# Performance work log

Hardware: AMD Instinct MI355X
Metric: run time of the kernel (lower is better)

The kernel has to match this reference:

```python
import jax, jax.numpy as jnp
import numpy as np

N_NODES = 50000


def gcn_conv(x, src, dst, norm, W, b, n_nodes):
    """One GCNConv layer: out = scatter_add(norm * (x @ W)[src] -> dst) + b.
    src/dst already include self loops; norm is the symmetric D^-1/2 A_hat D^-1/2 edge weight."""
    h = x @ W  # [N, C_out]
    msg = h[src] * norm[:, None]  # [E+N, C_out]
    out = jax.ops.segment_sum(msg, dst, num_segments=n_nodes)
    return out + b


def build_norm(edge_index, n_nodes):
    """Add self loops and compute symmetric GCN normalization (PyG GCNConv default)."""
    loop = jnp.arange(n_nodes, dtype=edge_index.dtype)
    src = jnp.concatenate([edge_index[0], loop])
    dst = jnp.concatenate([edge_index[1], loop])
    deg = jax.ops.segment_sum(jnp.ones_like(dst, dtype=jnp.float32), dst, num_segments=n_nodes)
    dinv = jnp.where(deg > 0, jax.lax.rsqrt(jnp.maximum(deg, 1.0)), 0.0)
    norm = dinv[src] * dinv[dst]
    return src, dst, norm


def setup_inputs() -> dict:
    key = jax.random.key(0)
    ks = jax.random.split(key, 8)
    in_c, h1, h2, out_c = 768, 256, 128, 2
    x = jax.random.normal(ks[0], (N_NODES, in_c), dtype=jnp.float32)
    edge_index = jax.random.randint(ks[1], (2, 800000), 0, N_NODES, dtype=jnp.int32)
    W1 = jax.random.normal(ks[2], (in_c, h1), dtype=jnp.float32) * 0.02
    b1 = jnp.zeros((h1,), dtype=jnp.float32)
    W2 = jax.random.normal(ks[3], (h1, h2), dtype=jnp.float32) * 0.02
    b2 = jnp.zeros((h2,), dtype=jnp.float32)
    W3 = jax.random.normal(ks[4], (h2, out_c), dtype=jnp.float32) * 0.02
    b3 = jnp.zeros((out_c,), dtype=jnp.float32)
    return {"x": x, "edge_index": edge_index, "W1": W1, "b1": b1,
            "W2": W2, "b2": b2, "W3": W3, "b3": b3}


def reference(x, edge_index, W1, b1, W2, b2, W3, b3):
    n = x.shape[0]
    src, dst, norm = build_norm(edge_index, n)
    # Dropout is identity in eval mode (training=False), so it is omitted.
    h = jax.nn.relu(gcn_conv(x, src, dst, norm, W1, b1, n))
    h = jax.nn.relu(gcn_conv(h, src, dst, norm, W2, b2, n))
    h = gcn_conv(h, src, dst, norm, W3, b3, n)
    return jax.nn.sigmoid(h)
```

## Files before the change

### kernel.cpp

```cpp
#include <hip/hip_runtime.h>
#include <math.h>

typedef short s16x8 __attribute__((ext_vector_type(8)));
typedef __bf16 b16x8 __attribute__((ext_vector_type(8)));
typedef float f32x4 __attribute__((ext_vector_type(4)));
typedef float f32x2 __attribute__((ext_vector_type(2)));
typedef unsigned int u32x4 __attribute__((ext_vector_type(4)));
typedef unsigned int u32x2 __attribute__((ext_vector_type(2)));

__device__ inline short f2bf(float f) {
    unsigned u = __float_as_uint(f);
    unsigned r = u + 0x7FFFu + ((u >> 16) & 1u);
    return (short)(r >> 16);
}
__device__ inline float bf2f(unsigned short u) {
    return __uint_as_float(((unsigned)u) << 16);
}


__global__ void count_kernel(const int* __restrict__ dst, int* __restrict__ cnt, int E) {
    int e = blockIdx.x * 256 + threadIdx.x;
    if (e < E) atomicAdd(&cnt[dst[e]], 1);
}


__device__ inline void make_wt_elem(const float* __restrict__ W, short* __restrict__ Wt,
                                    int K, int N, int idx) {
    int NB = N >> 7;
    int j = idx & 7;
    int l = (idx >> 3) & 63;
    int nt = (idx >> 9) & 7;
    int rest = idx >> 12;
    int b = rest % NB;
    int c = rest / NB;
    int k = c * 32 + (l >> 4) * 8 + j;
    int n = b * 128 + nt * 16 + (l & 15);
    Wt[idx] = f2bf(W[(size_t)k * N + n]);
}

__global__ __launch_bounds__(1024) void scanfix_kernel(
        const int* __restrict__ cnt, int* __restrict__ rp, int* __restrict__ cursor,
        float* __restrict__ dinv, int* __restrict__ bsum, int n, int E, int SB,
        const float* __restrict__ W1, short* __restrict__ Wt1,
        const float* __restrict__ W2, short* __restrict__ Wt2, int w1b) {
    int tid = threadIdx.x;
    if (blockIdx.x >= SB) {
        int b = blockIdx.x - SB;
        if (b < w1b) {
            int idx = b * 1024 + tid;
            make_wt_elem(W1, Wt1, 768, 256, idx);
        } else {
            int idx = (b - w1b) * 1024 + tid;
            make_wt_elem(W2, Wt2, 256, 128, idx);
        }
        return;
    }

    __shared__ int sdata[1024];
    __shared__ int parts[64];
    __shared__ int carry_s;
    int i = blockIdx.x * 1024 + tid;
    int v = (i < n) ? cnt[i] : 0;
    sdata[tid] = v;
    __syncthreads();
    for (int off = 1; off < 1024; off <<= 1) {
        int t = 0;
        if (tid >= off) t = sdata[tid - off];
        __syncthreads();
        sdata[tid] += t;
        __syncthreads();
    }
    if (tid == 1023)
        __hip_atomic_store(&bsum[blockIdx.x], sdata[1023] + 1,
                           __ATOMIC_RELEASE, __HIP_MEMORY_SCOPE_AGENT);
    int part = 0;
    if (tid < blockIdx.x) {
        int b;
        while ((b = __hip_atomic_load(&bsum[tid], __ATOMIC_ACQUIRE,
                                      __HIP_MEMORY_SCOPE_AGENT)) == 0) {}
        part = b - 1;
    }
    if (tid < 64) parts[tid] = part;
    __syncthreads();
    if (tid == 0) {
        int c = 0;
        for (int k = 0; k < 64; ++k) c += parts[k];
        carry_s = c;
    }
    __syncthreads();
    int r = sdata[tid] - v + carry_s;
    if (i < n) {
        rp[i] = r;
        cursor[i] = r;
        dinv[i] = rsqrtf((float)cnt[i] + 1.0f);
    }
    if (i == 0) rp[n] = E;
}


__global__ __launch_bounds__(256, 3) void gemm1_fill_kernel(
        const float* __restrict__ x, const short* __restrict__ Wt,
        unsigned char* __restrict__ h8, int M, int G1B, int FB,
        const int* __restrict__ src, const int* __restrict__ dst,
        int* __restrict__ cursor, const float* __restrict__ dinv,
        int2* __restrict__ ecw, int E) {
    constexpr int KC = 24;
    constexpr int RT = 2;
    constexpr int O = KC * 4;
    constexpr int F = KC * RT * 64 / 256;

    __shared__ s16x8 As[KC * RT * 64];

    const int tid = threadIdx.x;
    const int total = G1B + FB;
    const long long bi = (long long)blockIdx.x;
    const int fid  = (int)(bi * FB / total);
    const int fid1 = (int)((bi + 1) * FB / total);

    if (fid1 > fid) {
        int e = fid * 256 + tid;
        if (e < E) {
            int d = dst[e];
            int s = src[e];
            int p = atomicAdd(&cursor[d], 1);
            ecw[p] = make_int2(s, __float_as_int(dinv[s] * dinv[d]));
        }
        return;
    }
    const int gid = blockIdx.x - fid;

    const int m0 = gid * (RT * 16);

    s16x8 v[F];
#pragma unroll
    for (int i = 0; i < F; ++i) {
        int idx = i * 256 + tid;
        int r = idx / O;
        int o = idx - r * O;
        int row = m0 + r;
        if (row >= M) row = M - 1;
        const float4* fp = (const float4*)(x + (size_t)row * 768 + o * 8);
        float4 f0 = fp[0];
        float4 f1 = fp[1];
        u32x4 pk;
        pk.x = (__float_as_uint(f0.x) >> 16) | (__float_as_uint(f0.y) & 0xFFFF0000u);
        pk.y = (__float_as_uint(f0.z) >> 16) | (__float_as_uint(f0.w) & 0xFFFF0000u);
        pk.z = (__float_as_uint(f1.x) >> 16) | (__float_as_uint(f1.y) & 0xFFFF0000u);
        pk.w = (__float_as_uint(f1.z) >> 16) | (__float_as_uint(f1.w) & 0xFFFF0000u);
        v[i] = __builtin_bit_cast(s16x8, pk);
    }
#pragma unroll
    for (int i = 0; i < F; ++i) {
        int idx = i * 256 + tid;
        int r = idx / O;
        int o = idx - r * O;
        int c = o >> 2, q = o & 3;
        int slot = q * 16 + (((r & 15) + q + ((c & 3) << 2)) & 15);
        As[(c * RT + (r >> 4)) * 64 + slot] = v[i];
    }
    __syncthreads();

    const int lane = tid & 63;
    const int wave = tid >> 6;
    const int b128 = wave >> 1;
    const int nt0 = (wave & 1) * 4;
    const int q = lane >> 4;
    const int rl = lane & 15;
    const s16x8* wt = (const s16x8*)Wt;

    f32x4 acc[RT][4];
#pragma unroll
    for (int i = 0; i < RT; ++i)
#pragma unroll
        for (int j = 0; j < 4; ++j)
            acc[i][j] = (f32x4){0.f, 0.f, 0.f, 0.f};

#pragma unroll 4
    for (int c = 0; c < KC; ++c) {
        int slot = q * 16 + ((rl + q + ((c & 3) << 2)) & 15);
        b16x8 areg[RT], breg[4];
#pragma unroll
        for (int i = 0; i < RT; ++i)
            areg[i] = __builtin_bit_cast(b16x8, As[(c * RT + i) * 64 + slot]);
        size_t bb = (size_t)(c * 2 + b128) * 512 + nt0 * 64 + lane;
#pragma unroll
        for (int j = 0; j < 4; ++j)
            breg[j] = __builtin_bit_cast(b16x8, wt[bb + j * 64]);
#pragma unroll
        for (int i = 0; i < RT; ++i)
#pragma unroll
            for (int j = 0; j < 4; ++j)
                acc[i][j] = __builtin_amdgcn_mfma_f32_16x16x32_bf16(areg[i], breg[j], acc[i][j], 0, 0, 0);
    }

    const int quad = lane >> 4;
    const int nl = lane & 15;
#pragma unroll
    for (int i = 0; i < RT; ++i) {
        int rbase = m0 + i * 16 + quad * 4;
#pragma unroll
        for (int j = 0; j < 4; ++j) {
            int col = wave * 64 + j * 16 + nl;
#pragma unroll
            for (int r = 0; r < 4; ++r) {
                int row = rbase + r;
                if (row < M) {
                    unsigned u = __builtin_amdgcn_cvt_pk_fp8_f32(acc[i][j][r], acc[i][j][r], 0, false);
                    h8[(size_t)row * 256 + col] = (unsigned char)(u & 0xFF);
                }
            }
        }
    }
}


template<typename AT, int KC, int RT, int CW, int MINW, bool F8>
__global__ __launch_bounds__(256, MINW) void gemm_panel_kernel(
        const AT* __restrict__ A, const short* __restrict__ Wt,
        void* __restrict__ Cb, int M) {
    constexpr int K = KC * 32;
    constexpr int O = KC * 4;
    constexpr int F = KC * RT / 4;
    constexpr int NCOLS = CW * 64;
    constexpr int NB = NCOLS >> 7;
    constexpr int MT = RT * CW / 4;

    __shared__ s16x8 As[KC * RT * 64];

    const int tid = threadIdx.x;
    const int m0 = blockIdx.x * (RT * 16);

    s16x8 v[F];
#pragma unroll
    for (int i = 0; i < F; ++i) {
        int idx = i * 256 + tid;
        int r = idx / O;
        int o = idx - r * O;
        int row = m0 + r;
        if (row >= M) row = M - 1;
        v[i] = *(const s16x8*)((const unsigned short*)A + (size_t)row * K + o * 8);
    }
#pragma unroll
    for (int i = 0; i < F; ++i) {
        int idx = i * 256 + tid;
        int r = idx / O;
        int o = idx - r * O;
        int c = o >> 2, q = o & 3;
        int slot = q * 16 + (((r & 15) + q + ((c & 3) << 2)) & 15);
        As[(c * RT + (r >> 4)) * 64 + slot] = v[i];
    }
    __syncthreads();

    const int lane = tid & 63;
    const int wave = tid >> 6;
    const int cw_i = wave % CW;
    const int rg = wave / CW;
    const int mtb = rg * MT;
    const int b128 = (cw_i * 64) >> 7;
    const int nt0 = (cw_i * 4) & 7;
    const int q = lane >> 4;
    const int rl = lane & 15;
    const s16x8* wt = (const s16x8*)Wt;

    f32x4 acc[MT][4];
#pragma unroll
    for (int i = 0; i < MT; ++i)
#pragma unroll
        for (int j = 0; j < 4; ++j)
            acc[i][j] = (f32x4){0.f, 0.f, 0.f, 0.f};

#pragma unroll 4
    for (int c = 0; c < KC; ++c) {
        int slot = q * 16 + ((rl + q + ((c & 3) << 2)) & 15);
        b16x8 areg[MT], breg[4];
#pragma unroll
        for (int i = 0; i < MT; ++i)
            areg[i] = __builtin_bit_cast(b16x8, As[(c * RT + mtb + i) * 64 + slot]);
        size_t bb = (size_t)(c * NB + b128) * 512 + nt0 * 64 + lane;
#pragma unroll
        for (int j = 0; j < 4; ++j)
            breg[j] = __builtin_bit_cast(b16x8, wt[bb + j * 64]);
#pragma unroll
        for (int i = 0; i < MT; ++i)
#pragma unroll
            for (int j = 0; j < 4; ++j)
                acc[i][j] = __builtin_amdgcn_mfma_f32_16x16x32_bf16(areg[i], breg[j], acc[i][j], 0, 0, 0);
    }

    const int quad = lane >> 4;
    const int nl = lane & 15;
#pragma unroll
    for (int i = 0; i < MT; ++i) {
        int rbase = m0 + (mtb + i) * 16 + quad * 4;
#pragma unroll
        for (int j = 0; j < 4; ++j) {
            int col = cw_i * 64 + j * 16 + nl;
#pragma unroll
            for (int rr = 0; rr < 4; ++rr) {
                int row = rbase + rr;
                if (row < M) {
                    if (F8) {
                        unsigned u = __builtin_amdgcn_cvt_pk_fp8_f32(acc[i][j][rr], acc[i][j][rr], 0, false);
                        ((unsigned char*)Cb)[(size_t)row * NCOLS + col] = (unsigned char)(u & 0xFF);
                    } else {
                        ((unsigned short*)Cb)[(size_t)row * NCOLS + col] = (unsigned short)f2bf(acc[i][j][rr]);
                    }
                }
            }
        }
    }
}


__global__ __launch_bounds__(256) void agg256_f8_kernel(const unsigned char* __restrict__ h8,
                                                        const int* __restrict__ rp,
                                                        const int2* __restrict__ ecw,
                                                        const float* __restrict__ dinv,
                                                        const float* __restrict__ bias,
                                                        unsigned short* __restrict__ out, int n) {
    int node = blockIdx.x * 4 + (threadIdx.x >> 6);
    int lane = threadIdx.x & 63;
    if (node >= n) return;
    const int eg = lane >> 4;
    const int ch = lane & 15;
    float di = dinv[node];

    float acc[16];
    {
        u32x4 v = *(const u32x4*)(h8 + (size_t)node * 256 + ch * 16);
        float ws = (eg == 0) ? di * di : 0.f;
#pragma unroll
        for (int u = 0; u < 4; ++u) {
            f32x2 lo = __builtin_amdgcn_cvt_pk_f32_fp8(v[u], false);
            f32x2 hi = __builtin_amdgcn_cvt_pk_f32_fp8(v[u], true);
            acc[u * 4 + 0] = ws * lo.x; acc[u * 4 + 1] = ws * lo.y;
            acc[u * 4 + 2] = ws * hi.x; acc[u * 4 + 3] = ws * hi.y;
        }
    }

    int e0 = rp[node], e1 = rp[node + 1];
    for (int base = e0; base < e1; base += 64) {
        int idx = base + lane;
        int2 er = (idx < e1) ? ecw[idx] : make_int2(0, 0);
        int sb = er.x;
        float wb = __int_as_float(er.y);
        int cnt = e1 - base; if (cnt > 64) cnt = 64;
#pragma unroll 4
        for (int i = 0; i < cnt; i += 4) {
            int s = __shfl(sb, i + eg, 64);
            float w = __shfl(wb, i + eg, 64);
            u32x4 v = *(const u32x4*)(h8 + (size_t)s * 256 + ch * 16);
#pragma unroll
            for (int u = 0; u < 4; ++u) {
                f32x2 lo = __builtin_amdgcn_cvt_pk_f32_fp8(v[u], false);
                f32x2 hi = __builtin_amdgcn_cvt_pk_f32_fp8(v[u], true);
                acc[u * 4 + 0] += w * lo.x; acc[u * 4 + 1] += w * lo.y;
                acc[u * 4 + 2] += w * hi.x; acc[u * 4 + 3] += w * hi.y;
            }
        }
    }

#pragma unroll
    for (int k = 0; k < 16; ++k) {
        acc[k] += __shfl_xor(acc[k], 16, 64);
        acc[k] += __shfl_xor(acc[k], 32, 64);
    }

    unsigned pk[8];
#pragma unroll
    for (int k = 0; k < 8; ++k) {
        float b0 = bias[ch * 16 + 2 * k];
        float b1 = bias[ch * 16 + 2 * k + 1];
        float a0 = fmaxf(acc[2 * k] + b0, 0.f);
        float a1 = fmaxf(acc[2 * k + 1] + b1, 0.f);
        pk[k] = ((unsigned)(unsigned short)f2bf(a0)) | (((unsigned)(unsigned short)f2bf(a1)) << 16);
    }
    if (eg < 2) {
        u32x4 ov;
        ov.x = pk[eg * 4 + 0]; ov.y = pk[eg * 4 + 1];
        ov.z = pk[eg * 4 + 2]; ov.w = pk[eg * 4 + 3];
        *(u32x4*)((char*)out + (size_t)node * 512 + ch * 32 + eg * 16) = ov;
    }
}

__global__ __launch_bounds__(256) void agg128_w3_kernel(const unsigned char* __restrict__ h,
                                                        const int* __restrict__ rp,
                                                        const int2* __restrict__ ecw,
                                                        const float* __restrict__ dinv,
                                                        const float* __restrict__ b2,
                                                        const float* __restrict__ W3,
                                                        float* __restrict__ z, int n) {
    int node = blockIdx.x * 4 + (threadIdx.x >> 6);
    int lane = threadIdx.x & 63;
    if (node >= n) return;
    const int eg = lane >> 4;
    const int ch = lane & 15;
    float di = dinv[node];

    float acc[8];
    {
        u32x2 v = *(const u32x2*)(h + (size_t)node * 128 + ch * 8);
        float ws = (eg == 0) ? di * di : 0.f;
        f32x2 l0 = __builtin_amdgcn_cvt_pk_f32_fp8(v.x, false);
        f32x2 h0 = __builtin_amdgcn_cvt_pk_f32_fp8(v.x, true);
        f32x2 l1 = __builtin_amdgcn_cvt_pk_f32_fp8(v.y, false);
        f32x2 h1 = __builtin_amdgcn_cvt_pk_f32_fp8(v.y, true);
        acc[0] = ws * l0.x; acc[1] = ws * l0.y; acc[2] = ws * h0.x; acc[3] = ws * h0.y;
        acc[4] = ws * l1.x; acc[5] = ws * l1.y; acc[6] = ws * h1.x; acc[7] = ws * h1.y;
    }

    int e0 = rp[node], e1 = rp[node + 1];
    for (int base = e0; base < e1; base += 64) {
        int idx = base + lane;
        int2 er = (idx < e1) ? ecw[idx] : make_int2(0, 0);
        int sb = er.x;
        float wb = __int_as_float(er.y);
        int cnt = e1 - base; if (cnt > 64) cnt = 64;
#pragma unroll 4
        for (int i = 0; i < cnt; i += 4) {
            int s = __shfl(sb, i + eg, 64);
            float w = __shfl(wb, i + eg, 64);
            u32x2 v = *(const u32x2*)(h + (size_t)s * 128 + ch * 8);
            f32x2 l0 = __builtin_amdgcn_cvt_pk_f32_fp8(v.x, false);
            f32x2 h0 = __builtin_amdgcn_cvt_pk_f32_fp8(v.x, true);
            f32x2 l1 = __builtin_amdgcn_cvt_pk_f32_fp8(v.y, false);
            f32x2 h1 = __builtin_amdgcn_cvt_pk_f32_fp8(v.y, true);
            acc[0] += w * l0.x; acc[1] += w * l0.y; acc[2] += w * h0.x; acc[3] += w * h0.y;
            acc[4] += w * l1.x; acc[5] += w * l1.y; acc[6] += w * h1.x; acc[7] += w * h1.y;
        }
    }

#pragma unroll
    for (int k = 0; k < 8; ++k) {
        acc[k] += __shfl_xor(acc[k], 16, 64);
        acc[k] += __shfl_xor(acc[k], 32, 64);
    }

    float z0 = 0.f, z1 = 0.f;
#pragma unroll
    for (int k = 0; k < 8; ++k) {
        float a = fmaxf(acc[k] + b2[ch * 8 + k], 0.f);
        z0 += a * W3[(ch * 8 + k) * 2];
        z1 += a * W3[(ch * 8 + k) * 2 + 1];
    }
    for (int off = 8; off > 0; off >>= 1) {
        z0 += __shfl_xor(z0, off, 64);
        z1 += __shfl_xor(z1, off, 64);
    }
    if (lane == 0) {
        z[2 * (size_t)node] = z0;
        z[2 * (size_t)node + 1] = z1;
    }
}

__global__ __launch_bounds__(256) void agg3_kernel(const float* __restrict__ z,
                                                   const int* __restrict__ rp,
                                                   const int2* __restrict__ ecw,
                                                   const float* __restrict__ dinv,
                                                   const float* __restrict__ bias,
                                                   float* __restrict__ out, int n) {
    int node = blockIdx.x * 4 + (threadIdx.x >> 6);
    int lane = threadIdx.x & 63;
    if (node >= n) return;
    float a0 = 0.f, a1 = 0.f;
    int e0 = rp[node], e1 = rp[node + 1];
    for (int idx = e0 + lane; idx < e1; idx += 64) {
        int2 er = ecw[idx];
        float w = __int_as_float(er.y);
        float2 zz = *(const float2*)(z + 2 * (size_t)er.x);
        a0 += w * zz.x;
        a1 += w * zz.y;
    }
    for (int off = 32; off > 0; off >>= 1) {
        a0 += __shfl_xor(a0, off, 64);
        a1 += __shfl_xor(a1, off, 64);
    }
    if (lane == 0) {
        float di = dinv[node];
        float2 zn = *(const float2*)(z + 2 * (size_t)node);
        a0 += di * di * zn.x + bias[0];
        a1 += di * di * zn.y + bias[1];
        out[2 * (size_t)node]     = 1.f / (1.f + __expf(-a0));
        out[2 * (size_t)node + 1] = 1.f / (1.f + __expf(-a1));
    }
}


extern "C" void kernel_launch(void* const* d_in, const int* in_sizes, int n_in,
                              void* d_out, int out_size, void* d_ws, size_t ws_size,
                              hipStream_t stream) {
    const float* x  = (const float*)d_in[0];
    const int*   ei = (const int*)d_in[1];
    const float* W1 = (const float*)d_in[2];
    const float* b1 = (const float*)d_in[3];
    const float* W2 = (const float*)d_in[4];
    const float* b2 = (const float*)d_in[5];
    const float* W3 = (const float*)d_in[6];
    const float* b3 = (const float*)d_in[7];
    float* out = (float*)d_out;

    const int E  = in_sizes[1] / 2;
    const int C1 = in_sizes[3];
    const int C2 = in_sizes[5];
    const int K1 = in_sizes[2] / C1;
    const int N  = in_sizes[0] / K1;

    const int* srcv = ei;
    const int* dstv = ei + E;

    char* p = (char*)d_ws;
    auto carve = [&](size_t bytes) {
        char* r = p;
        p += (bytes + 255) & ~(size_t)255;
        return r;
    };
    int*   cnt    = (int*)carve((size_t)N * 4);
    int*   bsum   = (int*)carve(1024 * 4);
    int*   rp     = (int*)carve((size_t)(N + 1) * 4);
    int*   cursor = (int*)carve((size_t)N * 4);
    float* dinv   = (float*)carve((size_t)N * 4);
    int2*  ecw    = (int2*)carve((size_t)E * 8);
    short* Wt1    = (short*)carve((size_t)K1 * C1 * 2);
    short* Wt2    = (short*)carve((size_t)C1 * C2 * 2);
    unsigned char* h8 = (unsigned char*)carve((size_t)N * C1);
    unsigned short* hB = (unsigned short*)carve((size_t)N * C1 * 2);
    unsigned char* h2 = (unsigned char*)carve((size_t)N * C2);
    float* zbuf   = (float*)carve((size_t)N * 2 * 4);

    const int nb  = (N + 1023) / 1024;
    const int cb  = (E + 255) / 256;
    const int w1b = (K1 * C1) / 1024;
    const int w2b = (C1 * C2) / 1024;
    const int g1b = (N + 31) / 32;
    const int fb  = (E + 255) / 256;

    size_t cntpad = (((size_t)N * 4) + 255) & ~(size_t)255;
    hipMemsetAsync(cnt, 0, cntpad + 1024 * 4, stream);
    count_kernel<<<cb, 256, 0, stream>>>(dstv, cnt, E);
    scanfix_kernel<<<nb + w1b + w2b, 1024, 0, stream>>>(cnt, rp, cursor, dinv, bsum,
                                                        N, E, nb, W1, Wt1, W2, Wt2, w1b);

    gemm1_fill_kernel<<<g1b + fb, 256, 0, stream>>>(x, Wt1, h8, N, g1b, fb,
                                                    srcv, dstv, cursor, dinv, ecw, E);
    agg256_f8_kernel<<<(N + 3) / 4, 256, 0, stream>>>(h8, rp, ecw, dinv, b1, hB, N);

    gemm_panel_kernel<unsigned short, 8, 4, 2, 4, true><<<(N + 63) / 64, 256, 0, stream>>>(hB, Wt2, h2, N);
    agg128_w3_kernel<<<(N + 3) / 4, 256, 0, stream>>>(h2, rp, ecw, dinv, b2, W3, zbuf, N);

    agg3_kernel<<<(N + 3) / 4, 256, 0, stream>>>(zbuf, rp, ecw, dinv, b3, out, N);
}
```

Baseline: 404.0 us.

## Fuse layer-1 aggregation with layer-2 GEMM via shared-memory tile

Merges the 256-channel aggregation kernel with the following layer-2 GEMM. Each block aggregates 16 nodes, writes the bias+ReLU bf16 rows into a swizzled LDS tile, then runs MFMA against Wt2 and stores fp8 output directly. This drops the N×256 bf16 intermediate buffer's write and re-read and one kernel launch. In exchange, each wave now handles 4 nodes serially before the GEMM, which lowers the parallelism available to hide gather latency, and the GEMM uses small 16-row tiles that reload Wt2 per block.

```diff
diff --git a/kernel.cpp b/kernel.cpp
--- a/kernel.cpp
+++ b/kernel.cpp
@@ -12,9 +12,6 @@
     unsigned u = __float_as_uint(f);
     unsigned r = u + 0x7FFFu + ((u >> 16) & 1u);
     return (short)(r >> 16);
-}
-__device__ inline float bf2f(unsigned short u) {
-    return __uint_as_float(((unsigned)u) << 16);
 }
 
 
@@ -214,172 +211,118 @@
 }
 
 
-template<typename AT, int KC, int RT, int CW, int MINW, bool F8>
-__global__ __launch_bounds__(256, MINW) void gemm_panel_kernel(
-        const AT* __restrict__ A, const short* __restrict__ Wt,
-        void* __restrict__ Cb, int M) {
-    constexpr int K = KC * 32;
-    constexpr int O = KC * 4;
-    constexpr int F = KC * RT / 4;
-    constexpr int NCOLS = CW * 64;
-    constexpr int NB = NCOLS >> 7;
-    constexpr int MT = RT * CW / 4;
-
-    __shared__ s16x8 As[KC * RT * 64];
-
-    const int tid = threadIdx.x;
-    const int m0 = blockIdx.x * (RT * 16);
-
-    s16x8 v[F];
-#pragma unroll
-    for (int i = 0; i < F; ++i) {
-        int idx = i * 256 + tid;
-        int r = idx / O;
-        int o = idx - r * O;
-        int row = m0 + r;
-        if (row >= M) row = M - 1;
-        v[i] = *(const s16x8*)((const unsigned short*)A + (size_t)row * K + o * 8);
-    }
-#pragma unroll
-    for (int i = 0; i < F; ++i) {
-        int idx = i * 256 + tid;
-        int r = idx / O;
-        int o = idx - r * O;
-        int c = o >> 2, q = o & 3;
-        int slot = q * 16 + (((r & 15) + q + ((c & 3) << 2)) & 15);
-        As[(c * RT + (r >> 4)) * 64 + slot] = v[i];
-    }
-    __syncthreads();
-
-    const int lane = tid & 63;
-    const int wave = tid >> 6;
-    const int cw_i = wave % CW;
-    const int rg = wave / CW;
-    const int mtb = rg * MT;
-    const int b128 = (cw_i * 64) >> 7;
-    const int nt0 = (cw_i * 4) & 7;
-    const int q = lane >> 4;
-    const int rl = lane & 15;
-    const s16x8* wt = (const s16x8*)Wt;
-
-    f32x4 acc[MT][4];
-#pragma unroll
-    for (int i = 0; i < MT; ++i)
-#pragma unroll
-        for (int j = 0; j < 4; ++j)
-            acc[i][j] = (f32x4){0.f, 0.f, 0.f, 0.f};
-
-#pragma unroll 4
-    for (int c = 0; c < KC; ++c) {
-        int slot = q * 16 + ((rl + q + ((c & 3) << 2)) & 15);
-        b16x8 areg[MT], breg[4];
-#pragma unroll
-        for (int i = 0; i < MT; ++i)
-            areg[i] = __builtin_bit_cast(b16x8, As[(c * RT + mtb + i) * 64 + slot]);
-        size_t bb = (size_t)(c * NB + b128) * 512 + nt0 * 64 + lane;
-#pragma unroll
-        for (int j = 0; j < 4; ++j)
-            breg[j] = __builtin_bit_cast(b16x8, wt[bb + j * 64]);
-#pragma unroll
-        for (int i = 0; i < MT; ++i)
-#pragma unroll
-            for (int j = 0; j < 4; ++j)
-                acc[i][j] = __builtin_amdgcn_mfma_f32_16x16x32_bf16(areg[i], breg[j], acc[i][j], 0, 0, 0);
-    }
-
-    const int quad = lane >> 4;
-    const int nl = lane & 15;
-#pragma unroll
-    for (int i = 0; i < MT; ++i) {
-        int rbase = m0 + (mtb + i) * 16 + quad * 4;
-#pragma unroll
-        for (int j = 0; j < 4; ++j) {
-            int col = cw_i * 64 + j * 16 + nl;
-#pragma unroll
-            for (int rr = 0; rr < 4; ++rr) {
-                int row = rbase + rr;
-                if (row < M) {
-                    if (F8) {
-                        unsigned u = __builtin_amdgcn_cvt_pk_fp8_f32(acc[i][j][rr], acc[i][j][rr], 0, false);
-                        ((unsigned char*)Cb)[(size_t)row * NCOLS + col] = (unsigned char)(u & 0xFF);
-                    } else {
-                        ((unsigned short*)Cb)[(size_t)row * NCOLS + col] = (unsigned short)f2bf(acc[i][j][rr]);
-                    }
-                }
-            }
-        }
-    }
-}
-
-
-__global__ __launch_bounds__(256) void agg256_f8_kernel(const unsigned char* __restrict__ h8,
+__global__ __launch_bounds__(256) void agg256_g2_kernel(const unsigned char* __restrict__ h8,
                                                         const int* __restrict__ rp,
                                                         const int2* __restrict__ ecw,
                                                         const float* __restrict__ dinv,
                                                         const float* __restrict__ bias,
-                                                        unsigned short* __restrict__ out, int n) {
-    int node = blockIdx.x * 4 + (threadIdx.x >> 6);
-    int lane = threadIdx.x & 63;
-    if (node >= n) return;
+                                                        const short* __restrict__ Wt2,
+                                                        unsigned char* __restrict__ h2, int n) {
+    __shared__ s16x8 As[8 * 64];
+
+    const int tid = threadIdx.x;
+    const int lane = tid & 63;
+    const int wave = tid >> 6;
     const int eg = lane >> 4;
     const int ch = lane & 15;
-    float di = dinv[node];
-
-    float acc[16];
-    {
-        u32x4 v = *(const u32x4*)(h8 + (size_t)node * 256 + ch * 16);
-        float ws = (eg == 0) ? di * di : 0.f;
-#pragma unroll
-        for (int u = 0; u < 4; ++u) {
-            f32x2 lo = __builtin_amdgcn_cvt_pk_f32_fp8(v[u], false);
-            f32x2 hi = __builtin_amdgcn_cvt_pk_f32_fp8(v[u], true);
-            acc[u * 4 + 0] = ws * lo.x; acc[u * 4 + 1] = ws * lo.y;
-            acc[u * 4 + 2] = ws * hi.x; acc[u * 4 + 3] = ws * hi.y;
-        }
-    }
-
-    int e0 = rp[node], e1 = rp[node + 1];
-    for (int base = e0; base < e1; base += 64) {
-        int idx = base + lane;
-        int2 er = (idx < e1) ? ecw[idx] : make_int2(0, 0);
-        int sb = er.x;
-        float wb = __int_as_float(er.y);
-        int cnt = e1 - base; if (cnt > 64) cnt = 64;
+    const int nb0 = blockIdx.x * 16;
+
+    for (int t = 0; t < 4; ++t) {
+        const int r = wave * 4 + t;
+        const int node = nb0 + r;
+        float acc[16];
+#pragma unroll
+        for (int k = 0; k < 16; ++k) acc[k] = 0.f;
+
+        if (node < n) {
+            float di = dinv[node];
+            {
+                u32x4 v = *(const u32x4*)(h8 + (size_t)node * 256 + ch * 16);
+                float ws = (eg == 0) ? di * di : 0.f;
+#pragma unroll
+                for (int u = 0; u < 4; ++u) {
+                    f32x2 lo = __builtin_amdgcn_cvt_pk_f32_fp8(v[u], false);
+                    f32x2 hi = __builtin_amdgcn_cvt_pk_f32_fp8(v[u], true);
+                    acc[u * 4 + 0] = ws * lo.x; acc[u * 4 + 1] = ws * lo.y;
+                    acc[u * 4 + 2] = ws * hi.x; acc[u * 4 + 3] = ws * hi.y;
+                }
+            }
+            int e0 = rp[node], e1 = rp[node + 1];
+            for (int base = e0; base < e1; base += 64) {
+                int idx = base + lane;
+                int2 er = (idx < e1) ? ecw[idx] : make_int2(0, 0);
+                int sb = er.x;
+                float wb = __int_as_float(er.y);
+                int cnt = e1 - base; if (cnt > 64) cnt = 64;
 #pragma unroll 4
-        for (int i = 0; i < cnt; i += 4) {
-            int s = __shfl(sb, i + eg, 64);
-            float w = __shfl(wb, i + eg, 64);
-            u32x4 v = *(const u32x4*)(h8 + (size_t)s * 256 + ch * 16);
-#pragma unroll
-            for (int u = 0; u < 4; ++u) {
-                f32x2 lo = __builtin_amdgcn_cvt_pk_f32_fp8(v[u], false);
-                f32x2 hi = __builtin_amdgcn_cvt_pk_f32_fp8(v[u], true);
-                acc[u * 4 + 0] += w * lo.x; acc[u * 4 + 1] += w * lo.y;
-                acc[u * 4 + 2] += w * hi.x; acc[u * 4 + 3] += w * hi.y;
+                for (int i = 0; i < cnt; i += 4) {
+                    int s = __shfl(sb, i + eg, 64);
+                    float w = __shfl(wb, i + eg, 64);
+                    u32x4 v = *(const u32x4*)(h8 + (size_t)s * 256 + ch * 16);
+#pragma unroll
+                    for (int u = 0; u < 4; ++u) {
+                        f32x2 lo = __builtin_amdgcn_cvt_pk_f32_fp8(v[u], false);
+                        f32x2 hi = __builtin_amdgcn_cvt_pk_f32_fp8(v[u], true);
+                        acc[u * 4 + 0] += w * lo.x; acc[u * 4 + 1] += w * lo.y;
+                        acc[u * 4 + 2] += w * hi.x; acc[u * 4 + 3] += w * hi.y;
+                    }
+                }
             }
-        }
-    }
-
-#pragma unroll
-    for (int k = 0; k < 16; ++k) {
-        acc[k] += __shfl_xor(acc[k], 16, 64);
-        acc[k] += __shfl_xor(acc[k], 32, 64);
-    }
-
-    unsigned pk[8];
-#pragma unroll
-    for (int k = 0; k < 8; ++k) {
-        float b0 = bias[ch * 16 + 2 * k];
-        float b1 = bias[ch * 16 + 2 * k + 1];
-        float a0 = fmaxf(acc[2 * k] + b0, 0.f);
-        float a1 = fmaxf(acc[2 * k + 1] + b1, 0.f);
-        pk[k] = ((unsigned)(unsigned short)f2bf(a0)) | (((unsigned)(unsigned short)f2bf(a1)) << 16);
-    }
-    if (eg < 2) {
-        u32x4 ov;
-        ov.x = pk[eg * 4 + 0]; ov.y = pk[eg * 4 + 1];
-        ov.z = pk[eg * 4 + 2]; ov.w = pk[eg * 4 + 3];
-        *(u32x4*)((char*)out + (size_t)node * 512 + ch * 32 + eg * 16) = ov;
+#pragma unroll
+            for (int k = 0; k < 16; ++k) {
+                acc[k] += __shfl_xor(acc[k], 16, 64);
+                acc[k] += __shfl_xor(acc[k], 32, 64);
+            }
+#pragma unroll
+            for (int k = 0; k < 16; ++k)
+                acc[k] = fmaxf(acc[k] + bias[ch * 16 + k], 0.f);
+        }
+
+        if (eg < 2) {
+            s16x8 v;
+            int base = eg * 8;
+#pragma unroll
+            for (int k = 0; k < 8; ++k) v[k] = f2bf(acc[base + k]);
+            int o = 2 * ch + eg;
+            int c = o >> 2, q = o & 3;
+            int slot = q * 16 + ((r + q + ((c & 3) << 2)) & 15);
+            As[c * 64 + slot] = v;
+        }
+    }
+    __syncthreads();
+
+    const int q = lane >> 4;
+    const int rl = lane & 15;
+    const s16x8* wt = (const s16x8*)Wt2;
+
+    f32x4 acc2[2];
+    acc2[0] = (f32x4){0.f, 0.f, 0.f, 0.f};
+    acc2[1] = (f32x4){0.f, 0.f, 0.f, 0.f};
+
+#pragma unroll
+    for (int c = 0; c < 8; ++c) {
+        int slot = q * 16 + ((rl + q + ((c & 3) << 2)) & 15);
+        b16x8 areg = __builtin_bit_cast(b16x8, As[c * 64 + slot]);
+        size_t bb = (size_t)c * 512 + (wave * 2) * 64 + lane;
+        b16x8 b0 = __builtin_bit_cast(b16x8, wt[bb]);
+        b16x8 b1 = __builtin_bit_cast(b16x8, wt[bb + 64]);
+        acc2[0] = __builtin_amdgcn_mfma_f32_16x16x32_bf16(areg, b0, acc2[0], 0, 0, 0);
+        acc2[1] = __builtin_amdgcn_mfma_f32_16x16x32_bf16(areg, b1, acc2[1], 0, 0, 0);
+    }
+
+    const int quad = lane >> 4;
+    const int nl = lane & 15;
+#pragma unroll
+    for (int j = 0; j < 2; ++j) {
+        int col = (wave * 2 + j) * 16 + nl;
+#pragma unroll
+        for (int rr = 0; rr < 4; ++rr) {
+            int row = nb0 + quad * 4 + rr;
+            if (row < n) {
+                unsigned u = __builtin_amdgcn_cvt_pk_fp8_f32(acc2[j][rr], acc2[j][rr], 0, false);
+                h2[(size_t)row * 128 + col] = (unsigned char)(u & 0xFF);
+            }
+        }
     }
 }
 
@@ -523,7 +466,6 @@
     short* Wt1    = (short*)carve((size_t)K1 * C1 * 2);
     short* Wt2    = (short*)carve((size_t)C1 * C2 * 2);
     unsigned char* h8 = (unsigned char*)carve((size_t)N * C1);
-    unsigned short* hB = (unsigned short*)carve((size_t)N * C1 * 2);
     unsigned char* h2 = (unsigned char*)carve((size_t)N * C2);
     float* zbuf   = (float*)carve((size_t)N * 2 * 4);
 
@@ -542,9 +484,9 @@
 
     gemm1_fill_kernel<<<g1b + fb, 256, 0, stream>>>(x, Wt1, h8, N, g1b, fb,
                                                     srcv, dstv, cursor, dinv, ecw, E);
-    agg256_f8_kernel<<<(N + 3) / 4, 256, 0, stream>>>(h8, rp, ecw, dinv, b1, hB, N);
-
-    gemm_panel_kernel<unsigned short, 8, 4, 2, 4, true><<<(N + 63) / 64, 256, 0, stream>>>(hB, Wt2, h2, N);
+
+    agg256_g2_kernel<<<(N + 15) / 16, 256, 0, stream>>>(h8, rp, ecw, dinv, b1, Wt2, h2, N);
+
     agg128_w3_kernel<<<(N + 3) / 4, 256, 0, stream>>>(h2, rp, ecw, dinv, b2, W3, zbuf, N);
 
     agg3_kernel<<<(N + 3) / 4, 256, 0, stream>>>(zbuf, rp, ecw, dinv, b3, out, N);
```

New measurement: 419.3 us. +3.8%, slower.
